# Performance work log

Hardware: AMD Instinct MI355X
Metric: run time of the kernel (lower is better)

Reference implementation:

```python
import jax, jax.numpy as jnp
import numpy as np

D_MODEL, D_HIDDEN, D_OUTPUT = 512, 1024, 128

def setup_inputs() -> dict:
    key = jax.random.key(0)
    ks = jax.random.split(key, 6)
    enc = jax.random.normal(ks[0], (8, 256, D_MODEL), dtype=jnp.float32)
    dec = jax.random.normal(ks[1], (8, 64, D_MODEL), dtype=jnp.float32)
    s1 = 1.0 / np.sqrt(2 * D_MODEL)
    s2 = 1.0 / np.sqrt(D_HIDDEN)
    W1 = jax.random.uniform(ks[2], (2 * D_MODEL, D_HIDDEN), jnp.float32, -s1, s1)
    b1 = jax.random.uniform(ks[3], (D_HIDDEN,), jnp.float32, -s1, s1)
    W2 = jax.random.uniform(ks[4], (D_HIDDEN, D_OUTPUT), jnp.float32, -s2, s2)
    b2 = jax.random.uniform(ks[5], (D_OUTPUT,), jnp.float32, -s2, s2)
    return {"encoder_state": enc, "decoder_state": dec, "W1": W1, "b1": b1, "W2": W2, "b2": b2}

def reference(encoder_state, decoder_state, W1, b1, W2, b2):
    # Split first linear's weight into encoder/decoder halves: equivalent to
    # concat([enc, dec], -1) @ W1, but avoids materializing the (B,T,U,2d) tensor.
    W_enc, W_dec = W1[:D_MODEL], W1[D_MODEL:]
    enc_proj = jnp.einsum('btd,dh->bth', encoder_state, W_enc)   # (B,T,H)
    dec_proj = jnp.einsum('bud,dh->buh', decoder_state, W_dec)   # (B,U,H)
    hidden = jnp.tanh(enc_proj[:, :, None, :] + dec_proj[:, None, :, :] + b1)  # (B,T,U,H)
    out = jnp.einsum('btuh,ho->btuo', hidden, W2) + b2           # (B,T,U,O)
    return out
```

## Files before the change

kernel.cpp:

```cpp
#include <hip/hip_runtime.h>
#include <hip/hip_bf16.h>


typedef _Float16 f16x8 __attribute__((ext_vector_type(8)));
typedef _Float16 f16x2 __attribute__((ext_vector_type(2)));
typedef float    f32x4 __attribute__((ext_vector_type(4)));

#define C2L 2.8853900817779268f

__device__ __forceinline__ float fast_exp2(float x) { return __builtin_amdgcn_exp2f(x); }

__device__ __forceinline__ f16x2 pk_cvt(float x, float y) {
    auto r = __builtin_amdgcn_cvt_pkrtz(x, y);
    union { decltype(r) a; f16x2 b; } c; c.a = r; return c.b;
}

__device__ __forceinline__ f16x8 tanh8(f16x8 e, f16x8 d) {
    const f16x8 one = {1,1,1,1,1,1,1,1};
    const f16x8 two = {2,2,2,2,2,2,2,2};
    const f16x8 cap = {126,126,126,126,126,126,126,126};
    union { f16x8 v; _Float16 s[8]; } p, r;
    p.v = e * d + one;
    p.v = __builtin_elementwise_min(p.v, cap);
    #pragma unroll
    for (int i = 0; i < 4; ++i) {
        _Float16 q  = p.s[2*i] * p.s[2*i+1];
        _Float16 rq = __builtin_amdgcn_rcph(q);
        r.s[2*i]   = p.s[2*i+1] * rq;
        r.s[2*i+1] = p.s[2*i]   * rq;
    }
    return one - two * r.v;
}

__device__ __forceinline__ void stage16(const void* g, void* l) {
    __builtin_amdgcn_global_load_lds(
        (const __attribute__((address_space(1))) unsigned int*)g,
        (__attribute__((address_space(3))) unsigned int*)l, 16, 0, 0);
}

__global__ __launch_bounds__(1024) void transpose_both(
    const float* __restrict__ W1, const float* __restrict__ W2,
    _Float16* __restrict__ W1T, _Float16* __restrict__ W2T)
{
    __shared__ float tile[32][33];
    int bx = blockIdx.x;
    const float* src; _Float16* dst; int C, c0;
    if (bx < 32) { src = W1; dst = W1T; C = 1024; c0 = bx * 32; }
    else         { src = W2; dst = W2T; C = 128;  c0 = (bx - 32) * 32; }
    int r0 = blockIdx.y * 32;
    int tx = threadIdx.x, ty = threadIdx.y;
    tile[ty][tx] = src[(r0 + ty) * C + (c0 + tx)];
    __syncthreads();
    dst[(size_t)(c0 + ty) * 1024 + (r0 + tx)] = (_Float16)tile[tx][ty];
}

__global__ __launch_bounds__(256) void proj_exp(
    const float* __restrict__ enc,
    const float* __restrict__ dec,
    const _Float16* __restrict__ W1T,
    const float* __restrict__ b1,
    _Float16* __restrict__ Ep,
    _Float16* __restrict__ Dp)
{
    const int K = 512;
    int tid  = threadIdx.x;
    int w    = tid >> 6, lane = tid & 63;
    int quad = lane >> 4, l15 = lane & 15;
    int m_base = blockIdx.y * 64 + w * 16;
    int n_base = blockIdx.x * 64;

    bool is_enc = (m_base < 2048);
    const float* A = is_enc ? (enc + (size_t)(m_base + l15) * K)
                            : (dec + (size_t)(m_base - 2048 + l15) * K);
    int koff = is_enc ? 0 : 512;

    f32x4 acc[4] = {};
    for (int kc = 0; kc < K; kc += 32) {
        int k = kc + quad * 8;
        float4 a_lo = *reinterpret_cast<const float4*>(A + k);
        float4 a_hi = *reinterpret_cast<const float4*>(A + k + 4);
        union { f16x8 v; f16x2 h[4]; } a;
        a.h[0] = pk_cvt(a_lo.x, a_lo.y);
        a.h[1] = pk_cvt(a_lo.z, a_lo.w);
        a.h[2] = pk_cvt(a_hi.x, a_hi.y);
        a.h[3] = pk_cvt(a_hi.z, a_hi.w);
        #pragma unroll
        for (int f = 0; f < 4; ++f) {
            int n = n_base + f * 16 + l15;
            f16x8 b = *reinterpret_cast<const f16x8*>(W1T + n * 1024 + koff + k);
            acc[f] = __builtin_amdgcn_mfma_f32_16x16x32_f16(a.v, b, acc[f], 0, 0, 0);
        }
    }

    #pragma unroll
    for (int f = 0; f < 4; ++f) {
        int col = n_base + f * 16 + l15;
        float bv = is_enc ? b1[col] : 0.0f;
        #pragma unroll
        for (int v = 0; v < 4; ++v) {
            int row = m_base + quad * 4 + v;
            float val = fast_exp2(C2L * (acc[f][v] + bv));
            if (is_enc) Ep[(size_t)row * 1024 + col] = (_Float16)val;
            else        Dp[(size_t)(row - 2048) * 1024 + col] = (_Float16)val;
        }
    }
}

__global__ __launch_bounds__(256, 2) void joint_main(
    const _Float16* __restrict__ Ep,
    const _Float16* __restrict__ Dp,
    const _Float16* __restrict__ W2T,
    const float* __restrict__ b2,
    float* __restrict__ out)
{
    __shared__ _Float16 sB[2][128 * 64];
    __shared__ _Float16 sE[4 * 1024];

    int t0 = blockIdx.x * 4, b = blockIdx.y;
    int tid  = threadIdx.x;
    int w    = tid >> 6, lane = tid & 63;
    int quad = lane >> 4, l15 = lane & 15;
    int u0   = w * 16;

    const _Float16* epB = Ep + (size_t)(b * 256 + t0) * 1024;
    const _Float16* dpr = Dp + (size_t)(b * 64 + u0 + l15) * 1024;

    f32x4 acc[4][8] = {};

    #pragma unroll
    for (int i = 0; i < 2; ++i) {
        int c = i * 256 + tid;
        stage16(epB + c * 8, sE + (i * 256 + (tid & 0xC0)) * 8);
    }
    #pragma unroll
    for (int i = 0; i < 4; ++i) {
        int c = i * 256 + tid;
        int row = c >> 3, kcs = c & 7;
        stage16(W2T + row * 1024 + ((kcs ^ (row & 7)) << 3),
                &sB[0][(i * 256 + (tid & 0xC0)) * 8]);
    }

    for (int it = 0; it < 16; ++it) {
        __syncthreads();
        if (it < 15) {
            int kb = (it + 1) * 64;
            _Float16* dst = sB[(it + 1) & 1];
            #pragma unroll
            for (int i = 0; i < 4; ++i) {
                int c = i * 256 + tid;
                int row = c >> 3, kcs = c & 7;
                stage16(W2T + row * 1024 + kb + ((kcs ^ (row & 7)) << 3),
                        dst + (i * 256 + (tid & 0xC0)) * 8);
            }
        }
        const _Float16* sb = sB[it & 1];
        #pragma unroll
        for (int ki2 = 0; ki2 < 2; ++ki2) {
            int k = it * 64 + ki2 * 32 + quad * 8;
            f16x8 d8 = *reinterpret_cast<const f16x8*>(dpr + k);
            f16x8 A[4];
            #pragma unroll
            for (int tt = 0; tt < 4; ++tt) {
                f16x8 e = *reinterpret_cast<const f16x8*>(sE + tt * 1024 + k);
                A[tt] = tanh8(e, d8);
            }
            int kc3 = ki2 * 4 + quad;
            int sw  = (kc3 ^ (l15 & 7)) << 3;
            #pragma unroll
            for (int f = 0; f < 8; ++f) {
                f16x8 bb = *reinterpret_cast<const f16x8*>(
                    sb + (f * 16 + l15) * 64 + sw);
                #pragma unroll
                for (int tt = 0; tt < 4; ++tt)
                    acc[tt][f] = __builtin_amdgcn_mfma_f32_16x16x32_f16(A[tt], bb, acc[tt][f], 0, 0, 0);
            }
        }
    }

    #pragma unroll
    for (int tt = 0; tt < 4; ++tt) {
        float* o = out + (size_t)(b * 256 + t0 + tt) * 64 * 128;
        #pragma unroll
        for (int f = 0; f < 8; ++f) {
            int oc = f * 16 + l15;
            float bv = b2[oc];
            #pragma unroll
            for (int v = 0; v < 4; ++v) {
                int u = u0 + quad * 4 + v;
                o[u * 128 + oc] = acc[tt][f][v] + bv;
            }
        }
    }
}

extern "C" void kernel_launch(void* const* d_in, const int* in_sizes, int n_in,
                              void* d_out, int out_size, void* d_ws, size_t ws_size,
                              hipStream_t stream) {
    const float* enc = (const float*)d_in[0];
    const float* dec = (const float*)d_in[1];
    const float* W1  = (const float*)d_in[2];
    const float* b1  = (const float*)d_in[3];
    const float* W2  = (const float*)d_in[4];
    const float* b2  = (const float*)d_in[5];
    float* out = (float*)d_out;

    char* ws = (char*)d_ws;
    _Float16* W1T = (_Float16*)(ws);
    _Float16* W2T = (_Float16*)(ws + (2u << 20));
    _Float16* EpP = (_Float16*)(ws + (2u << 20) + (256u << 10));
    _Float16* DpP = (_Float16*)(ws + (6u << 20) + (256u << 10));

    transpose_both<<<dim3(36, 32), dim3(32, 32), 0, stream>>>(W1, W2, W1T, W2T);

    proj_exp<<<dim3(16, 40), 256, 0, stream>>>(enc, dec, W1T, b1, EpP, DpP);

    joint_main<<<dim3(64, 8), 256, 0, stream>>>(EpP, DpP, W2T, b2, out);
}
```

Before: 155.9 us.

## Stage decoder projections in LDS, rotate K order, vectorize weight transpose

```diff
diff --git a/kernel.cpp b/kernel.cpp
--- a/kernel.cpp
+++ b/kernel.cpp
@@ -38,20 +38,33 @@
         (__attribute__((address_space(3))) unsigned int*)l, 16, 0, 0);
 }
 
-__global__ __launch_bounds__(1024) void transpose_both(
+__global__ __launch_bounds__(256) void transpose_both(
     const float* __restrict__ W1, const float* __restrict__ W2,
     _Float16* __restrict__ W1T, _Float16* __restrict__ W2T)
 {
-    __shared__ float tile[32][33];
-    int bx = blockIdx.x;
-    const float* src; _Float16* dst; int C, c0;
-    if (bx < 32) { src = W1; dst = W1T; C = 1024; c0 = bx * 32; }
-    else         { src = W2; dst = W2T; C = 128;  c0 = (bx - 32) * 32; }
-    int r0 = blockIdx.y * 32;
-    int tx = threadIdx.x, ty = threadIdx.y;
-    tile[ty][tx] = src[(r0 + ty) * C + (c0 + tx)];
+    __shared__ float tile[64][65];
+    int bi = blockIdx.x;
+    const float* src; _Float16* dst; int C, r0, c0;
+    if (bi < 256) { src = W1; dst = W1T; C = 1024; r0 = (bi >> 4) << 6; c0 = (bi & 15) << 6; }
+    else { int b2i = bi - 256; src = W2; dst = W2T; C = 128; r0 = (b2i >> 1) << 6; c0 = (b2i & 1) << 6; }
+    int t = threadIdx.x;
+    #pragma unroll
+    for (int i = 0; i < 4; ++i) {
+        int c = i * 256 + t;
+        int row = c >> 4, c4 = (c & 15) << 2;
+        *reinterpret_cast<float4*>(&tile[row][c4]) =
+            *reinterpret_cast<const float4*>(src + (size_t)(r0 + row) * C + c0 + c4);
+    }
     __syncthreads();
-    dst[(size_t)(c0 + ty) * 1024 + (r0 + tx)] = (_Float16)tile[tx][ty];
+    #pragma unroll
+    for (int i = 0; i < 2; ++i) {
+        int d = i * 256 + t;
+        int cc = d >> 3, rj = (d & 7) << 3;
+        f16x8 v;
+        #pragma unroll
+        for (int e = 0; e < 8; ++e) v[e] = (_Float16)tile[rj + e][cc];
+        *reinterpret_cast<f16x8*>(dst + (size_t)(c0 + cc) * 1024 + r0 + rj) = v;
+    }
 }
 
 __global__ __launch_bounds__(256) void proj_exp(
@@ -113,7 +126,8 @@
     const float* __restrict__ b2,
     float* __restrict__ out)
 {
-    __shared__ _Float16 sB[2][128 * 64];
+    __shared__ _Float16 sW[2][128 * 64];
+    __shared__ _Float16 sD[2][64 * 64];
     __shared__ _Float16 sE[4 * 1024];
 
     int t0 = blockIdx.x * 4, b = blockIdx.y;
@@ -121,9 +135,10 @@
     int w    = tid >> 6, lane = tid & 63;
     int quad = lane >> 4, l15 = lane & 15;
     int u0   = w * 16;
+    int rot  = ((blockIdx.y >> 2) & 1) << 3;
 
     const _Float16* epB = Ep + (size_t)(b * 256 + t0) * 1024;
-    const _Float16* dpr = Dp + (size_t)(b * 64 + u0 + l15) * 1024;
+    const _Float16* dpB = Dp + (size_t)(b * 64) * 1024;
 
     f32x4 acc[4][8] = {};
 
@@ -132,48 +147,73 @@
         int c = i * 256 + tid;
         stage16(epB + c * 8, sE + (i * 256 + (tid & 0xC0)) * 8);
     }
-    #pragma unroll
-    for (int i = 0; i < 4; ++i) {
-        int c = i * 256 + tid;
-        int row = c >> 3, kcs = c & 7;
-        stage16(W2T + row * 1024 + ((kcs ^ (row & 7)) << 3),
-                &sB[0][(i * 256 + (tid & 0xC0)) * 8]);
-    }
-
-    for (int it = 0; it < 16; ++it) {
+    {
+        int kb = rot * 64;
+        #pragma unroll
+        for (int i = 0; i < 4; ++i) {
+            int c = i * 256 + tid;
+            int row = c >> 3, kcs = c & 7;
+            stage16(W2T + row * 1024 + kb + ((kcs ^ (row & 7)) << 3),
+                    &sW[0][(i * 256 + (tid & 0xC0)) * 8]);
+        }
+        #pragma unroll
+        for (int i = 0; i < 2; ++i) {
+            int c = i * 256 + tid;
+            int row = c >> 3, kcs = c & 7;
+            stage16(dpB + row * 1024 + kb + ((kcs ^ (row & 7)) << 3),
+                    &sD[0][(i * 256 + (tid & 0xC0)) * 8]);
+        }
+    }
+
+    int rowu = u0 + l15;
+    int rx   = rowu & 7;
+
+    for (int ii = 0; ii < 16; ++ii) {
+        int it = (ii + rot) & 15;
         __syncthreads();
-        if (it < 15) {
-            int kb = (it + 1) * 64;
-            _Float16* dst = sB[(it + 1) & 1];
+        if (ii < 15) {
+            int kb = (((ii + 1) + rot) & 15) * 64;
+            _Float16* dw = sW[(ii + 1) & 1];
+            _Float16* dd = sD[(ii + 1) & 1];
             #pragma unroll
             for (int i = 0; i < 4; ++i) {
                 int c = i * 256 + tid;
                 int row = c >> 3, kcs = c & 7;
                 stage16(W2T + row * 1024 + kb + ((kcs ^ (row & 7)) << 3),
-                        dst + (i * 256 + (tid & 0xC0)) * 8);
-            }
-        }
-        const _Float16* sb = sB[it & 1];
+                        dw + (i * 256 + (tid & 0xC0)) * 8);
+            }
+            #pragma unroll
+            for (int i = 0; i < 2; ++i) {
+                int c = i * 256 + tid;
+                int row = c >> 3, kcs = c & 7;
+                stage16(dpB + row * 1024 + kb + ((kcs ^ (row & 7)) << 3),
+                        dd + (i * 256 + (tid & 0xC0)) * 8);
+            }
+        }
+        const _Float16* sw = sW[ii & 1];
+        const _Float16* sd = sD[ii & 1];
         #pragma unroll
         for (int ki2 = 0; ki2 < 2; ++ki2) {
-            int k = it * 64 + ki2 * 32 + quad * 8;
-            f16x8 d8 = *reinterpret_cast<const f16x8*>(dpr + k);
+            int kc3 = ki2 * 4 + quad;
+            f16x8 d8 = *reinterpret_cast<const f16x8*>(sd + rowu * 64 + ((kc3 ^ rx) << 3));
+            int kq = it * 64 + ki2 * 32 + quad * 8;
             f16x8 A[4];
             #pragma unroll
             for (int tt = 0; tt < 4; ++tt) {
-                f16x8 e = *reinterpret_cast<const f16x8*>(sE + tt * 1024 + k);
+                f16x8 e = *reinterpret_cast<const f16x8*>(sE + tt * 1024 + kq);
                 A[tt] = tanh8(e, d8);
             }
-            int kc3 = ki2 * 4 + quad;
-            int sw  = (kc3 ^ (l15 & 7)) << 3;
+            int swo = (kc3 ^ (l15 & 7)) << 3;
+            __builtin_amdgcn_s_setprio(1);
             #pragma unroll
             for (int f = 0; f < 8; ++f) {
                 f16x8 bb = *reinterpret_cast<const f16x8*>(
-                    sb + (f * 16 + l15) * 64 + sw);
+                    sw + (f * 16 + l15) * 64 + swo);
                 #pragma unroll
                 for (int tt = 0; tt < 4; ++tt)
                     acc[tt][f] = __builtin_amdgcn_mfma_f32_16x16x32_f16(A[tt], bb, acc[tt][f], 0, 0, 0);
             }
+            __builtin_amdgcn_s_setprio(0);
         }
     }
 
@@ -210,7 +250,7 @@
     _Float16* EpP = (_Float16*)(ws + (2u << 20) + (256u << 10));
     _Float16* DpP = (_Float16*)(ws + (6u << 20) + (256u << 10));
 
-    transpose_both<<<dim3(36, 32), dim3(32, 32), 0, stream>>>(W1, W2, W1T, W2T);
+    transpose_both<<<dim3(288), dim3(256), 0, stream>>>(W1, W2, W1T, W2T);
 
     proj_exp<<<dim3(16, 40), 256, 0, stream>>>(enc, dec, W1T, b1, EpP, DpP);
 
```

New measurement: 161.3 us. 1.03x slower.
